# Kernel tuning notes

Hardware: AMD Instinct MI355X
Metric: run time of the kernel (lower is better)

## Reference

```python
import jax, jax.numpy as jnp
import numpy as np
from jax import lax

WINDOW = 512
HOP = 128
SR = 16000
ALPHA = 1e-06
F = WINDOW // 2 + 1  # 257 bins
GAIN = float(np.sqrt(8.0 / 3.0))

# frequency-domain constants (match PsychoacousticMasker properties)
_freqs = np.linspace(0.0, SR / 2.0, F)
_bark_np = 13.0 * np.arctan(0.00076 * _freqs) + 3.5 * np.arctan((_freqs / 7500.0) ** 2)
_valid_dom = (_freqs >= 20.0) & (_freqs <= 20000.0)
_ath_np = np.full(F, -np.inf)
_fk = _freqs[_valid_dom] * 0.001
_ath_np[_valid_dom] = 3.64 * _fk ** -0.8 - 6.5 * np.exp(-0.6 * (_fk - 3.3) ** 2) + 0.001 * _fk ** 4 - 12.0
BARK = jnp.asarray(_bark_np, jnp.float32)
ATH = jnp.asarray(_ath_np, jnp.float32)
DELTA_SHIFT = -6.025 - 0.275 * BARK
HANN = jnp.asarray(0.5 * (1.0 - np.cos(2.0 * np.pi * np.arange(WINDOW) / WINDOW)), jnp.float32)


def _stft(x):
    # center=False hann STFT -> [n_frames, F] complex
    n_frames = (x.shape[0] - WINDOW) // HOP + 1
    idx = jnp.arange(n_frames)[:, None] * HOP + jnp.arange(WINDOW)[None, :]
    return jnp.fft.rfft(x[idx] * HANN, axis=-1)


def _frame_threshold(p):
    # p: [F] SPL-normalized PSD (dB) for one frame -> global masking threshold [F]
    interior = (p[1:-1] > p[:-2]) & (p[1:-1] > p[2:])
    is_max = jnp.pad(interior, (1, 1), constant_values=False)
    pw = 10.0 ** (p / 10.0)
    m_all = 10.0 * jnp.log10(pw + jnp.roll(pw, 1) + jnp.roll(pw, -1))  # tonal masker level (bins j-1,j,j+1)
    valid = is_max & (m_all > ATH)
    order = jnp.argsort((~valid).astype(jnp.int32))  # stable: valid bins first, in frequency order
    vmask = valid[order]
    m_c = jnp.where(vmask, m_all[order], -200.0)     # compacted masker dB values
    n = valid.sum()

    def step(carry, i):
        i_prev, keep = carry
        active = i < n
        # NB: source indexes bark[] with masker *list positions* (i, i_prev); replicated faithfully
        close = (BARK[i] - BARK[i_prev]) < 0.5
        prev_smaller = m_c[i_prev] < m_c[i]
        del_idx = jnp.where(prev_smaller, i_prev, i)
        keep = jnp.where(active & close, keep.at[del_idx].set(False), keep)
        i_prev = jnp.where(active, jnp.where(close, jnp.where(prev_smaller, i_prev + 1, i_prev), i), i_prev)
        return (i_prev, keep), None

    (_, keep), _ = lax.scan(step, (jnp.int32(0), jnp.ones(F, dtype=bool)), jnp.arange(1, F, dtype=jnp.int32))
    keep = keep & vmask
    # individual thresholds, vectorized over maskers k and bins
    z_j = BARK[order]                                    # bark of each masker's bin
    dz = BARK[None, :] - z_j[:, None]                    # [K, F]
    slope = jnp.where(dz > 0, -27.0 + 0.37 * jnp.maximum(m_c - 40.0, 0.0)[:, None], 27.0)
    t = m_c[:, None] + DELTA_SHIFT[order][:, None] + slope * dz
    power = jnp.where(keep[:, None], 10.0 ** (t / 10.0), 0.0)
    return 10.0 * jnp.log10(power.sum(0) + 10.0 ** (ATH / 10.0))


def _threshold_and_psd_max(audio):
    s = _stft(audio)                                     # [T, F]
    psd = 20.0 * jnp.log10(jnp.abs(GAIN * s / WINDOW))
    psd = jnp.maximum(psd, -200.0)
    psd_max = psd.max()
    psd_n = 96.0 - psd_max + psd
    thr = jax.vmap(_frame_threshold)(psd_n)              # [T, F]
    return thr, psd_max


def setup_inputs() -> dict:
    key = jax.random.key(0)
    k1, k2 = jax.random.split(key)
    L = 160000  # 10 s @ 16 kHz; (L - 512) % 128 == 0 -> 1247 frames, pad is a no-op
    x_ref = 0.5 * jax.random.normal(k1, (L,), dtype=jnp.float32)
    x_adv = x_ref + 0.01 * jax.random.normal(k2, (L,), dtype=jnp.float32)
    return {"x_adv": x_adv, "x_ref": x_ref}


def reference(x_adv, x_ref):
    thr, psd_max = _threshold_and_psd_max(x_ref)
    thr = lax.stop_gradient(thr)
    psd_max = lax.stop_gradient(psd_max)
    delta = x_adv - x_ref
    sd = _stft(delta)                                    # [T, F]
    psd_d = (GAIN / WINDOW) ** 2 * (sd.real ** 2 + sd.imag ** 2)
    psd_d = (10.0 ** 9.6) / (10.0 ** (psd_max / 10.0)) * psd_d
    loss = jnp.mean(jax.nn.relu(psd_d - 10.0 ** (thr / 10.0)))
    return ALPHA * loss
```

## Files before the change

### kernel.cpp

```cpp
#include <hip/hip_runtime.h>
#include <math.h>


#define FBINS 257

#define TAB_BARK  0
#define TAB_ATHDB 257
#define TAB_ATHP  514
#define TAB_HANN  771
#define TAB_TWR   1283
#define TAB_TWI   1539
#define TAB_FLOATS 2048

__global__ __launch_bounds__(256) void k0_init(float* __restrict__ tab)
{
    const int tid = threadIdx.x;
    const double TWO_PI = 6.283185307179586476925286766559;
    for (int f = tid; f < FBINS; f += 256) {
        double freq = 31.25 * (double)f;
        double q    = freq / 7500.0;
        tab[TAB_BARK + f] = (float)(13.0 * atan(0.00076 * freq) + 3.5 * atan(q * q));
        if (f == 0) {
            tab[TAB_ATHDB] = -INFINITY;
            tab[TAB_ATHP]  = 0.0f;
        } else {
            double fk = freq * 0.001;
            double ad = 3.64 * pow(fk, -0.8)
                      - 6.5 * exp(-0.6 * (fk - 3.3) * (fk - 3.3))
                      + 0.001 * fk * fk * fk * fk - 12.0;
            float av = (float)ad;
            tab[TAB_ATHDB + f] = av;
            tab[TAB_ATHP  + f] = exp10f(av / 10.0f);
        }
    }
    for (int n = tid; n < 512; n += 256) {
        double cw = cos((TWO_PI * (double)n) / 512.0);
        tab[TAB_HANN + n] = (float)(0.5 * (1.0 - cw));
    }
    for (int j = tid; j < 256; j += 256) {
        double s, c;
        sincos(-(TWO_PI / 512.0) * (double)j, &s, &c);
        tab[TAB_TWR + j] = (float)c;
        tab[TAB_TWI + j] = (float)s;
    }
}

__global__ __launch_bounds__(256) void k1_stft(
    const float* __restrict__ xadv, const float* __restrict__ xref,
    const float* __restrict__ tab,
    float* __restrict__ psd_db, float* __restrict__ pd, float* __restrict__ fmaxs)
{
    __shared__ float re[512], im[512], twr[256], twi[256];
    __shared__ float wmax[4];
    const int t = blockIdx.x, tid = threadIdx.x;

    twr[tid] = tab[TAB_TWR + tid];
    twi[tid] = tab[TAB_TWI + tid];

    const int base_idx = t * 128;
    for (int n = tid; n < 512; n += 256) {
        float w = tab[TAB_HANN + n];
        float r = xref[base_idx + n];
        float a = xadv[base_idx + n];
        int   p = __brev((unsigned)n) >> 23;
        re[p] = w * r;
        im[p] = w * (a - r);
    }
    __syncthreads();

    for (int stage = 1; stage <= 9; ++stage) {
        int half  = 1 << (stage - 1);
        int tstep = 512 >> stage;
        int j     = tid & (half - 1);
        int base  = ((tid >> (stage - 1)) << stage) + j;
        float wr = twr[j * tstep], wi = twi[j * tstep];
        float vr0 = re[base + half], vi0 = im[base + half];
        float vr = vr0 * wr - vi0 * wi;
        float vi = vr0 * wi + vi0 * wr;
        float ur = re[base], ui = im[base];
        __syncthreads();
        re[base]        = ur + vr; im[base]        = ui + vi;
        re[base + half] = ur - vr; im[base + half] = ui - vi;
        __syncthreads();
    }

    const float S2 = 1.0172526041666667e-05f;
    float lmax = -1e30f;
    for (int k = tid; k <= 256; k += 256) {
        int nk = (512 - k) & 511;
        float zr = re[k],  zi = im[k];
        float yr = re[nk], yi = im[nk];
        float ar = 0.5f * (zr + yr), ai = 0.5f * (zi - yi);
        float br = 0.5f * (zi + yi), bi = 0.5f * (yr - zr);
        float prefp = S2 * (ar * ar + ai * ai);
        float pdb   = fmaxf(10.0f * log10f(prefp), -200.0f);
        psd_db[t * FBINS + k] = pdb;
        pd[t * FBINS + k]     = S2 * (br * br + bi * bi);
        lmax = fmaxf(lmax, pdb);
    }
    for (int off = 32; off > 0; off >>= 1) lmax = fmaxf(lmax, __shfl_down(lmax, off));
    if ((tid & 63) == 0) wmax[tid >> 6] = lmax;
    __syncthreads();
    if (tid == 0)
        fmaxs[t] = fmaxf(fmaxf(wmax[0], wmax[1]), fmaxf(wmax[2], wmax[3]));
}

__global__ __launch_bounds__(256) void k2_max(
    const float* __restrict__ fmaxs, int nf, float* __restrict__ psdmax)
{
    __shared__ float sm[4];
    float v = -1e30f;
    for (int i = threadIdx.x; i < nf; i += 256) v = fmaxf(v, fmaxs[i]);
    for (int off = 32; off > 0; off >>= 1) v = fmaxf(v, __shfl_down(v, off));
    if ((threadIdx.x & 63) == 0) sm[threadIdx.x >> 6] = v;
    __syncthreads();
    if (threadIdx.x == 0)
        psdmax[0] = fmaxf(fmaxf(sm[0], sm[1]), fmaxf(sm[2], sm[3]));
}

__global__ __launch_bounds__(256) void k3_threshold(
    const float* __restrict__ tab,
    const float* __restrict__ psd_db, const float* __restrict__ pd,
    const float* __restrict__ psdmax, float* __restrict__ floss)
{
    __shared__ float barkf[FBINS], athp_s[FBINS];
    __shared__ float p_s[FBINS], pw_s[FBINS];
    __shared__ float mc_s[128], shift_s[128], barkm_s[128], ups_s[128];
    __shared__ int   bin_s[128], keep_s[128];
    __shared__ int   wcnt[4];
    __shared__ float red[4];

    const int t = blockIdx.x, tid = threadIdx.x;
    const int lane = tid & 63, wid = tid >> 6;
    const float pmax   = psdmax[0];
    const float shift0 = 96.0f - pmax;

    for (int f = tid; f < FBINS; f += 256) {
        barkf[f]  = tab[TAB_BARK + f];
        athp_s[f] = tab[TAB_ATHP + f];
        float pv = shift0 + psd_db[t * FBINS + f];
        p_s[f]  = pv;
        pw_s[f] = exp10f(pv / 10.0f);
    }
    __syncthreads();

    float m = -1e30f;
    int   pred = 0;
    if (tid >= 1 && tid <= 255) {
        float pc = p_s[tid];
        if (pc > p_s[tid - 1] && pc > p_s[tid + 1]) {
            m = 10.0f * log10f((pw_s[tid] + pw_s[tid - 1]) + pw_s[tid + 1]);
            if (m > tab[TAB_ATHDB + tid]) pred = 1;
        }
    }
    unsigned long long bal = __ballot(pred);
    if (lane == 0) wcnt[wid] = __popcll(bal);
    __syncthreads();
    int base = 0;
    for (int w = 0; w < wid; ++w) base += wcnt[w];
    const int n_total = wcnt[0] + wcnt[1] + wcnt[2] + wcnt[3];
    if (pred) {
        int pos = base + __popcll(bal & ((1ull << lane) - 1));
        bin_s[pos] = tid; mc_s[pos] = m; keep_s[pos] = 1;
    }
    __syncthreads();

    if (tid == 0) {
        int i_prev = 0;
        for (int i = 1; i < n_total; ++i) {
            bool close        = (barkf[i] - barkf[i_prev]) < 0.5f;
            bool prev_smaller = mc_s[i_prev] < mc_s[i];
            if (close) {
                keep_s[prev_smaller ? i_prev : i] = 0;
                if (prev_smaller) i_prev = i_prev + 1;
            } else {
                i_prev = i;
            }
        }
    }
    __syncthreads();

    int pred2 = (tid < n_total) && keep_s[tid];
    unsigned long long bal2 = __ballot(pred2);
    if (lane == 0) wcnt[wid] = __popcll(bal2);
    __syncthreads();
    int base2 = 0;
    for (int w = 0; w < wid; ++w) base2 += wcnt[w];
    const int nk = wcnt[0] + wcnt[1] + wcnt[2] + wcnt[3];
    if (pred2) {
        int pos = base2 + __popcll(bal2 & ((1ull << lane) - 1));
        int   fb = bin_s[tid];
        float mc = mc_s[tid];
        shift_s[pos] = mc + (-6.025f - 0.275f * barkf[fb]);
        barkm_s[pos] = barkf[fb];
        ups_s[pos]   = -27.0f + 0.37f * fmaxf(mc - 40.0f, 0.0f);
    }
    __syncthreads();

    const float C = 3981071705.534973f / exp10f(pmax / 10.0f);
    float lsum = 0.0f;
    for (int f = tid; f < FBINS; f += 256) {
        float bf  = barkf[f];
        float acc = 0.0f;
        for (int k = 0; k < nk; ++k) {
            float dz    = bf - barkm_s[k];
            float slope = (dz > 0.0f) ? ups_s[k] : 27.0f;
            float tdb   = shift_s[k] + slope * dz;
            acc += exp10f(tdb / 10.0f);
        }
        float thrpow = acc + athp_s[f];
        float pds    = C * pd[t * FBINS + f];
        lsum += fmaxf(pds - thrpow, 0.0f);
    }
    for (int off = 32; off > 0; off >>= 1) lsum += __shfl_down(lsum, off);
    if ((tid & 63) == 0) red[tid >> 6] = lsum;
    __syncthreads();
    if (tid == 0) floss[t] = (red[0] + red[1]) + (red[2] + red[3]);
}

__global__ __launch_bounds__(256) void k4_final(
    const float* __restrict__ floss, int nf, float* __restrict__ out)
{
    __shared__ float red[4];
    float s = 0.0f;
    for (int i = threadIdx.x; i < nf; i += 256) s += floss[i];
    for (int off = 32; off > 0; off >>= 1) s += __shfl_down(s, off);
    if ((threadIdx.x & 63) == 0) red[threadIdx.x >> 6] = s;
    __syncthreads();
    if (threadIdx.x == 0) {
        float total = (red[0] + red[1]) + (red[2] + red[3]);
        out[0] = 1e-6f * (total / (float)(nf * FBINS));
    }
}

extern "C" void kernel_launch(void* const* d_in, const int* in_sizes, int n_in,
                              void* d_out, int out_size, void* d_ws, size_t ws_size,
                              hipStream_t stream)
{
    const float* x_adv = (const float*)d_in[0];
    const float* x_ref = (const float*)d_in[1];
    float*       out   = (float*)d_out;

    const int L  = in_sizes[0];
    const int nf = (L - 512) / 128 + 1;

    float* ws      = (float*)d_ws;
    float* tab     = ws;
    float* psd_db  = ws + TAB_FLOATS;
    float* pd      = psd_db + (size_t)nf * FBINS;
    float* fmaxs   = pd + (size_t)nf * FBINS;
    float* floss   = fmaxs + nf;
    float* psdmax  = floss + nf;

    k0_init     <<<1,  256, 0, stream>>>(tab);
    k1_stft     <<<nf, 256, 0, stream>>>(x_adv, x_ref, tab, psd_db, pd, fmaxs);
    k2_max      <<<1,  256, 0, stream>>>(fmaxs, nf, psdmax);
    k3_threshold<<<nf, 256, 0, stream>>>(tab, psd_db, pd, psdmax, floss);
    k4_final    <<<1,  256, 0, stream>>>(floss, nf, out);
}
```

Before: 93.87 us.

## Fold max and final reductions into atomics, ping-pong FFT, speed serial suppression

Drops the two single-block reduction kernels. The global PSD max is now computed with an order-preserving atomicMax from each STFT block, and the final loss sum is done by the last-arriving threshold block, found through an atomic counter. The FFT uses ping-pong shared buffers so each butterfly stage needs one barrier instead of two. The serial masker-suppression loop reads values through readlane from registers, using precomputed bark-closeness bounds, instead of shared-memory loads. This removes two launches and shortens the serial path, in exchange for atomic contention and a slightly changed summation order.

Result: slower. 120.5 us (+28.4%).

```diff
diff --git a/kernel.cpp b/kernel.cpp
--- a/kernel.cpp
+++ b/kernel.cpp
@@ -10,7 +10,24 @@
 #define TAB_HANN  771
 #define TAB_TWR   1283
 #define TAB_TWI   1539
+#define TAB_PSDMAX 1800
+#define TAB_COUNT  1801
 #define TAB_FLOATS 2048
+
+__device__ inline unsigned enc_f(float f) {
+    unsigned u = __float_as_uint(f);
+    return (u & 0x80000000u) ? ~u : (u | 0x80000000u);
+}
+__device__ inline float dec_f(unsigned k) {
+    return (k & 0x80000000u) ? __uint_as_float(k & 0x7fffffffu)
+                             : __uint_as_float(~k);
+}
+__device__ inline float rl_f(float v, int l) {
+    return __int_as_float(__builtin_amdgcn_readlane(__float_as_int(v), l));
+}
+__device__ inline int rl_i(int v, int l) {
+    return __builtin_amdgcn_readlane(v, l);
+}
 
 __global__ __launch_bounds__(256) void k0_init(float* __restrict__ tab)
 {
@@ -37,20 +54,25 @@
         double cw = cos((TWO_PI * (double)n) / 512.0);
         tab[TAB_HANN + n] = (float)(0.5 * (1.0 - cw));
     }
-    for (int j = tid; j < 256; j += 256) {
+    if (tid < 256) {
         double s, c;
-        sincos(-(TWO_PI / 512.0) * (double)j, &s, &c);
-        tab[TAB_TWR + j] = (float)c;
-        tab[TAB_TWI + j] = (float)s;
-    }
-}
-
-__global__ __launch_bounds__(256) void k1_stft(
+        sincos(-(TWO_PI / 512.0) * (double)tid, &s, &c);
+        tab[TAB_TWR + tid] = (float)c;
+        tab[TAB_TWI + tid] = (float)s;
+    }
+    if (tid == 0) {
+        ((unsigned*)tab)[TAB_PSDMAX] = 0u;
+        ((unsigned*)tab)[TAB_COUNT]  = 0u;
+    }
+}
+
+__global__ __launch_bounds__(256) void kA_stft(
     const float* __restrict__ xadv, const float* __restrict__ xref,
     const float* __restrict__ tab,
-    float* __restrict__ psd_db, float* __restrict__ pd, float* __restrict__ fmaxs)
+    float* __restrict__ psd_db, float* __restrict__ pd, unsigned* __restrict__ psdmax_u)
 {
-    __shared__ float re[512], im[512], twr[256], twi[256];
+    __shared__ float reA[512], imA[512], reB[512], imB[512];
+    __shared__ float twr[256], twi[256];
     __shared__ float wmax[4];
     const int t = blockIdx.x, tid = threadIdx.x;
 
@@ -63,76 +85,79 @@
         float r = xref[base_idx + n];
         float a = xadv[base_idx + n];
         int   p = __brev((unsigned)n) >> 23;
-        re[p] = w * r;
-        im[p] = w * (a - r);
-    }
-    __syncthreads();
-
+        reA[p] = w * r;
+        imA[p] = w * (a - r);
+    }
+    __syncthreads();
+
+    float *rs = reA, *is = imA, *rd = reB, *id = imB;
     for (int stage = 1; stage <= 9; ++stage) {
         int half  = 1 << (stage - 1);
         int tstep = 512 >> stage;
         int j     = tid & (half - 1);
         int base  = ((tid >> (stage - 1)) << stage) + j;
         float wr = twr[j * tstep], wi = twi[j * tstep];
-        float vr0 = re[base + half], vi0 = im[base + half];
+        float vr0 = rs[base + half], vi0 = is[base + half];
         float vr = vr0 * wr - vi0 * wi;
         float vi = vr0 * wi + vi0 * wr;
-        float ur = re[base], ui = im[base];
-        __syncthreads();
-        re[base]        = ur + vr; im[base]        = ui + vi;
-        re[base + half] = ur - vr; im[base + half] = ui - vi;
+        float ur = rs[base], ui = is[base];
+        rd[base]        = ur + vr; id[base]        = ui + vi;
+        rd[base + half] = ur - vr; id[base + half] = ui - vi;
+        float* tp;
+        tp = rs; rs = rd; rd = tp;
+        tp = is; is = id; id = tp;
         __syncthreads();
     }
 
     const float S2 = 1.0172526041666667e-05f;
     float lmax = -1e30f;
-    for (int k = tid; k <= 256; k += 256) {
+    {
+        int k  = tid;
         int nk = (512 - k) & 511;
-        float zr = re[k],  zi = im[k];
-        float yr = re[nk], yi = im[nk];
+        float zr = rs[k],  zi = is[k];
+        float yr = rs[nk], yi = is[nk];
         float ar = 0.5f * (zr + yr), ai = 0.5f * (zi - yi);
         float br = 0.5f * (zi + yi), bi = 0.5f * (yr - zr);
         float prefp = S2 * (ar * ar + ai * ai);
         float pdb   = fmaxf(10.0f * log10f(prefp), -200.0f);
         psd_db[t * FBINS + k] = pdb;
         pd[t * FBINS + k]     = S2 * (br * br + bi * bi);
-        lmax = fmaxf(lmax, pdb);
+        lmax = pdb;
+        if (tid == 0) {
+            float zr2 = rs[256], zi2 = is[256];
+            float prefp2 = S2 * (zr2 * zr2);
+            float pdb2   = fmaxf(10.0f * log10f(prefp2), -200.0f);
+            psd_db[t * FBINS + 256] = pdb2;
+            pd[t * FBINS + 256]     = S2 * (zi2 * zi2);
+            lmax = fmaxf(lmax, pdb2);
+        }
     }
     for (int off = 32; off > 0; off >>= 1) lmax = fmaxf(lmax, __shfl_down(lmax, off));
     if ((tid & 63) == 0) wmax[tid >> 6] = lmax;
     __syncthreads();
-    if (tid == 0)
-        fmaxs[t] = fmaxf(fmaxf(wmax[0], wmax[1]), fmaxf(wmax[2], wmax[3]));
-}
-
-__global__ __launch_bounds__(256) void k2_max(
-    const float* __restrict__ fmaxs, int nf, float* __restrict__ psdmax)
-{
-    __shared__ float sm[4];
-    float v = -1e30f;
-    for (int i = threadIdx.x; i < nf; i += 256) v = fmaxf(v, fmaxs[i]);
-    for (int off = 32; off > 0; off >>= 1) v = fmaxf(v, __shfl_down(v, off));
-    if ((threadIdx.x & 63) == 0) sm[threadIdx.x >> 6] = v;
-    __syncthreads();
-    if (threadIdx.x == 0)
-        psdmax[0] = fmaxf(fmaxf(sm[0], sm[1]), fmaxf(sm[2], sm[3]));
-}
-
-__global__ __launch_bounds__(256) void k3_threshold(
+    if (tid == 0) {
+        float m = fmaxf(fmaxf(wmax[0], wmax[1]), fmaxf(wmax[2], wmax[3]));
+        atomicMax(psdmax_u, enc_f(m));
+    }
+}
+
+__global__ __launch_bounds__(256) void kB_threshold(
     const float* __restrict__ tab,
     const float* __restrict__ psd_db, const float* __restrict__ pd,
-    const float* __restrict__ psdmax, float* __restrict__ floss)
+    const unsigned* __restrict__ psdmax_u, unsigned* __restrict__ counter,
+    float* __restrict__ floss, float* __restrict__ out, int nf)
 {
     __shared__ float barkf[FBINS], athp_s[FBINS];
     __shared__ float p_s[FBINS], pw_s[FBINS];
     __shared__ float mc_s[128], shift_s[128], barkm_s[128], ups_s[128];
-    __shared__ int   bin_s[128], keep_s[128];
+    __shared__ int   bin_s[128], keep_s[128], qmax_s[128];
     __shared__ int   wcnt[4];
     __shared__ float red[4];
+    __shared__ int   amLast;
 
     const int t = blockIdx.x, tid = threadIdx.x;
     const int lane = tid & 63, wid = tid >> 6;
-    const float pmax   = psdmax[0];
+    const float pmax   = dec_f(psdmax_u[0]);
     const float shift0 = 96.0f - pmax;
 
     for (int f = tid; f < FBINS; f += 256) {
@@ -155,6 +180,11 @@
     }
     unsigned long long bal = __ballot(pred);
     if (lane == 0) wcnt[wid] = __popcll(bal);
+    if (tid < 128) {
+        int q = tid;
+        while (q + 1 < FBINS && (barkf[q + 1] - barkf[tid]) < 0.5f) ++q;
+        qmax_s[tid] = q;
+    }
     __syncthreads();
     int base = 0;
     for (int w = 0; w < wid; ++w) base += wcnt[w];
@@ -165,16 +195,31 @@
     }
     __syncthreads();
 
-    if (tid == 0) {
-        int i_prev = 0;
+    float mcw0 = 0.0f, mcw1 = 0.0f;
+    int   qmw0 = 0,    qmw1 = 0;
+    if (wid == 0) {
+        mcw0 = mc_s[lane];        mcw1 = mc_s[lane + 64];
+        qmw0 = qmax_s[lane];      qmw1 = qmax_s[lane + 64];
+    }
+    if (tid == 0 && n_total > 1) {
+        int   i_prev = 0;
+        float mcp = rl_f(mcw0, 0);
+        int   qmp = rl_i(qmw0, 0);
         for (int i = 1; i < n_total; ++i) {
-            bool close        = (barkf[i] - barkf[i_prev]) < 0.5f;
-            bool prev_smaller = mc_s[i_prev] < mc_s[i];
+            float mci = (i < 64) ? rl_f(mcw0, i) : rl_f(mcw1, i - 64);
+            bool close = (i <= qmp);
+            bool ps    = mcp < mci;
             if (close) {
-                keep_s[prev_smaller ? i_prev : i] = 0;
-                if (prev_smaller) i_prev = i_prev + 1;
+                keep_s[ps ? i_prev : i] = 0;
+                if (ps) {
+                    i_prev += 1;
+                    mcp = (i_prev < 64) ? rl_f(mcw0, i_prev) : rl_f(mcw1, i_prev - 64);
+                    qmp = (i_prev < 64) ? rl_i(qmw0, i_prev) : rl_i(qmw1, i_prev - 64);
+                }
             } else {
                 i_prev = i;
+                mcp = mci;
+                qmp = (i < 64) ? rl_i(qmw0, i) : rl_i(qmw1, i - 64);
             }
         }
     }
@@ -215,21 +260,25 @@
     for (int off = 32; off > 0; off >>= 1) lsum += __shfl_down(lsum, off);
     if ((tid & 63) == 0) red[tid >> 6] = lsum;
     __syncthreads();
-    if (tid == 0) floss[t] = (red[0] + red[1]) + (red[2] + red[3]);
-}
-
-__global__ __launch_bounds__(256) void k4_final(
-    const float* __restrict__ floss, int nf, float* __restrict__ out)
-{
-    __shared__ float red[4];
-    float s = 0.0f;
-    for (int i = threadIdx.x; i < nf; i += 256) s += floss[i];
-    for (int off = 32; off > 0; off >>= 1) s += __shfl_down(s, off);
-    if ((threadIdx.x & 63) == 0) red[threadIdx.x >> 6] = s;
-    __syncthreads();
-    if (threadIdx.x == 0) {
-        float total = (red[0] + red[1]) + (red[2] + red[3]);
-        out[0] = 1e-6f * (total / (float)(nf * FBINS));
+    if (tid == 0) {
+        floss[t] = (red[0] + red[1]) + (red[2] + red[3]);
+        __threadfence();
+        unsigned old = atomicAdd(counter, 1u);
+        amLast = (old == (unsigned)(gridDim.x - 1));
+    }
+    __syncthreads();
+
+    if (amLast) {
+        __threadfence();
+        float s = 0.0f;
+        for (int i = tid; i < nf; i += 256) s += floss[i];
+        for (int off = 32; off > 0; off >>= 1) s += __shfl_down(s, off);
+        if ((tid & 63) == 0) red[tid >> 6] = s;
+        __syncthreads();
+        if (tid == 0) {
+            float total = (red[0] + red[1]) + (red[2] + red[3]);
+            out[0] = 1e-6f * (total / (float)(nf * FBINS));
+        }
     }
 }
 
@@ -248,13 +297,12 @@
     float* tab     = ws;
     float* psd_db  = ws + TAB_FLOATS;
     float* pd      = psd_db + (size_t)nf * FBINS;
-    float* fmaxs   = pd + (size_t)nf * FBINS;
-    float* floss   = fmaxs + nf;
-    float* psdmax  = floss + nf;
+    float* floss   = pd + (size_t)nf * FBINS;
+    unsigned* psdmax_u = (unsigned*)tab + TAB_PSDMAX;
+    unsigned* counter  = (unsigned*)tab + TAB_COUNT;
 
     k0_init     <<<1,  256, 0, stream>>>(tab);
-    k1_stft     <<<nf, 256, 0, stream>>>(x_adv, x_ref, tab, psd_db, pd, fmaxs);
-    k2_max      <<<1,  256, 0, stream>>>(fmaxs, nf, psdmax);
-    k3_threshold<<<nf, 256, 0, stream>>>(tab, psd_db, pd, psdmax, floss);
-    k4_final    <<<1,  256, 0, stream>>>(floss, nf, out);
-}
+    kA_stft     <<<nf, 256, 0, stream>>>(x_adv, x_ref, tab, psd_db, pd, psdmax_u);
+    kB_threshold<<<nf, 256, 0, stream>>>(tab, psd_db, pd, psdmax_u, counter,
+                                         floss, out, nf);
+}
```
